# Kernel optimization log

Measured on AMD Instinct MI355X. Metric: run time of the kernel, lower is better.

Reference implementation:

```python
import jax, jax.numpy as jnp
import numpy as np

B, S, D, H = 2, 2048, 1024, 16
HD = D // H


def setup_inputs() -> dict:
    key = jax.random.key(0)
    ks = jax.random.split(key, 5)
    x = jax.random.normal(ks[0], (B, S, D), dtype=jnp.float32)
    qk_w = jax.random.normal(ks[1], (D, 2 * D), dtype=jnp.float32) * 0.02
    qk_b = jnp.zeros((2 * D,), dtype=jnp.float32)
    v_w = jax.random.normal(ks[2], (D, D), dtype=jnp.float32) * 0.02
    cproj_w = jax.random.normal(ks[3], (D, D), dtype=jnp.float32) * 0.02
    resid_gain = jnp.ones((1, H, 1, 1), dtype=jnp.float32)
    skip_gain = jnp.ones((1, H, 1, 1), dtype=jnp.float32)
    centre_gain = jnp.ones((1, H, 1, 1), dtype=jnp.float32)
    return {"x": x, "qk_w": qk_w, "qk_b": qk_b, "v_w": v_w,
            "cproj_w": cproj_w, "resid_gain": resid_gain,
            "skip_gain": skip_gain, "centre_gain": centre_gain}


def reference(x, qk_w, qk_b, v_w, cproj_w, resid_gain, skip_gain, centre_gain):
    b, s, d = x.shape
    h, hd = H, d // H
    # fused QK projection (pconv with bias)
    qk = x @ qk_w + qk_b                      # [B,S,2D]
    q, k = jnp.split(qk, 2, axis=-1)
    v = x @ v_w                               # [B,S,D] (pconv, bias=0)
    # split heads -> [B,H,S,hd]
    q = q.reshape(b, s, h, hd).transpose(0, 2, 1, 3)
    k = k.reshape(b, s, h, hd).transpose(0, 2, 1, 3)
    v = v.reshape(b, s, h, hd).transpose(0, 2, 1, 3)
    # scaled QK^T with causal mask
    scores = jnp.einsum('bhqd,bhkd->bhqk', q, k) / jnp.sqrt(jnp.float32(hd))
    causal = jnp.tril(jnp.ones((s, s), dtype=bool))
    neg = jnp.finfo(scores.dtype).min
    scores = jnp.where(causal, scores, neg)
    attn = jax.nn.softmax(scores, axis=-1)    # [B,H,S,S]
    # shaped attention: per-head resid gain + skip (identity) - centred uniform causal
    row = jnp.arange(1, s + 1, dtype=jnp.float32)
    uniform = jnp.tril(jnp.ones((s, s), dtype=jnp.float32) / row[:, None])  # [S,S]
    eye = jnp.eye(s, dtype=jnp.float32)
    new_attn = (resid_gain * attn
                + skip_gain * eye[None, None]
                - centre_gain * uniform[None, None])
    out = jnp.einsum('bhqk,bhkd->bhqd', new_attn, v)  # [B,H,S,hd]
    out = out.transpose(0, 2, 1, 3).reshape(b, s, d)  # merge heads
    out = out @ cproj_w                                # c_proj (bias=0)
    return out
```

## Files before the change

kernel.cpp:

```cpp
#include <hip/hip_runtime.h>
#include <hip/hip_bf16.h>


typedef __hip_bfloat16 bf16;
typedef short s16x8 __attribute__((ext_vector_type(8)));
typedef short s16x4 __attribute__((ext_vector_type(4)));
typedef float f32x4 __attribute__((ext_vector_type(4)));

#define NB 2
#define NS 2048
#define ND 1024
#define NH 16
#define NHD 64
#define QSCALE 0.18033688011112042f
#define THR 8.0f
#define SW(r) (((r) & 7) << 4)

__device__ __forceinline__ float b2f(unsigned short u) {
  union { float f; unsigned int i; } c; c.i = ((unsigned int)u) << 16; return c.f;
}

__device__ __forceinline__ unsigned short f2bu(float f) {
  bf16 t = __float2bfloat16(f);
  unsigned short u;
  __builtin_memcpy(&u, &t, 2);
  return u;
}

__device__ __forceinline__ void gload_lds16(const void* g, void* l) {
  __builtin_amdgcn_global_load_lds((const __attribute__((address_space(1))) void*)g,
                                   (__attribute__((address_space(3))) void*)l, 16, 0, 0);
}

__global__ __launch_bounds__(256) void cvt_bf16(const float* __restrict__ in,
                                                bf16* __restrict__ out, int n4) {
  int i = blockIdx.x * 256 + threadIdx.x;
  if (i >= n4) return;
  float4 v = ((const float4*)in)[i];
  ushort4 o;
  o.x = f2bu(v.x); o.y = f2bu(v.y); o.z = f2bu(v.z); o.w = f2bu(v.w);
  ((ushort4*)out)[i] = o;
}

__global__ __launch_bounds__(256) void tconv3(const float* __restrict__ qk_w,
                                              const float* __restrict__ v_w,
                                              const float* __restrict__ cp_w,
                                              bf16* __restrict__ qkwt,
                                              bf16* __restrict__ vwt,
                                              bf16* __restrict__ cpwt) {
  const int z = blockIdx.z;
  const int N = (z == 0) ? 2048 : 1024;
  if (blockIdx.x * 32 >= N) return;
  const float* in = (z == 0) ? qk_w : (z == 1) ? v_w : cp_w;
  bf16* out = (z == 0) ? qkwt : (z == 1) ? vwt : cpwt;
  const int K = 1024;
  __shared__ float tile[32][33];
  int nt = blockIdx.x * 32, kt = blockIdx.y * 32;
  int tx = threadIdx.x, ty = threadIdx.y;
#pragma unroll
  for (int j = 0; j < 32; j += 8)
    tile[ty + j][tx] = in[(size_t)(kt + ty + j) * N + nt + tx];
  __syncthreads();
#pragma unroll
  for (int j = 0; j < 32; j += 8)
    out[(size_t)(nt + ty + j) * K + kt + tx] = __float2bfloat16(tile[tx][ty + j]);
}

__global__ __launch_bounds__(256) void gemm_qkv(const bf16* __restrict__ A,
                                                const bf16* __restrict__ BtQK,
                                                const bf16* __restrict__ BtV,
                                                const float* __restrict__ bias,
                                                bf16* __restrict__ qo, bf16* __restrict__ ko,
                                                bf16* __restrict__ vo) {
  __shared__ alignas(16) bf16 As[128 * 32];
  __shared__ alignas(16) bf16 Bs[128 * 32];
  const int K = 1024;
  const int tid = threadIdx.x;
  const int wave = tid >> 6, lane = tid & 63;
  const int l15 = lane & 15, lg = lane >> 4;
  const int wr = wave >> 1, wc = wave & 1;
  const int brow = blockIdx.y * 128, bcol = blockIdx.x * 128;
  const bf16* Bsrc = (bcol < 2048) ? (BtQK + (size_t)bcol * K)
                                   : (BtV + (size_t)(bcol - 2048) * K);

  f32x4 acc[4][4] = {};
  const int r0 = tid >> 2;
  const int kc = (tid & 3) * 8;
  char* AsB = (char*)As;
  char* BsB = (char*)Bs;

  for (int k0 = 0; k0 < K; k0 += 32) {
    gload_lds16(A + (size_t)(brow + r0) * K + k0 + kc, AsB + tid * 16);
    gload_lds16(A + (size_t)(brow + r0 + 64) * K + k0 + kc, AsB + 4096 + tid * 16);
    gload_lds16(Bsrc + (size_t)r0 * K + k0 + kc, BsB + tid * 16);
    gload_lds16(Bsrc + (size_t)(r0 + 64) * K + k0 + kc, BsB + 4096 + tid * 16);
    __syncthreads();
    s16x8 af[4], bfr[4];
#pragma unroll
    for (int mi = 0; mi < 4; ++mi)
      af[mi] = *(const s16x8*)(As + (wr * 64 + mi * 16 + l15) * 32 + lg * 8);
#pragma unroll
    for (int ni = 0; ni < 4; ++ni)
      bfr[ni] = *(const s16x8*)(Bs + (wc * 64 + ni * 16 + l15) * 32 + lg * 8);
#pragma unroll
    for (int mi = 0; mi < 4; ++mi)
#pragma unroll
      for (int ni = 0; ni < 4; ++ni)
        acc[mi][ni] = __builtin_amdgcn_mfma_f32_16x16x32_bf16(af[mi], bfr[ni], acc[mi][ni], 0, 0, 0);
    __syncthreads();
  }

#pragma unroll
  for (int mi = 0; mi < 4; ++mi)
#pragma unroll
    for (int ni = 0; ni < 4; ++ni)
#pragma unroll
      for (int r = 0; r < 4; ++r) {
        int row = brow + wr * 64 + mi * 16 + lg * 4 + r;
        int col = bcol + wc * 64 + ni * 16 + l15;
        float v = acc[mi][ni][r];
        int b = row >> 11, s = row & 2047;
        int cc = col & 1023;
        int h = cc >> 6, e = cc & 63;
        if (col < 1024) {
          v = (v + bias[col]) * QSCALE;
          qo[((((size_t)b * NH + h) * NS) + s) * NHD + e] = __float2bfloat16(v);
        } else if (col < 2048) {
          v += bias[col];
          ko[((((size_t)b * NH + h) * NS) + s) * NHD + e] = __float2bfloat16(v);
        } else {
          vo[((((size_t)b * NH + h) * NHD) + e) * NS + s] = __float2bfloat16(v);
        }
      }
}

__global__ __launch_bounds__(256) void gemm_out(const bf16* __restrict__ A,
                                                const bf16* __restrict__ Bt,
                                                float* __restrict__ of) {
  __shared__ alignas(16) bf16 As[128 * 32];
  __shared__ alignas(16) bf16 Bs[64 * 32];
  const int K = 1024, N = 1024;
  const int tid = threadIdx.x;
  const int wave = tid >> 6, lane = tid & 63;
  const int l15 = lane & 15, lg = lane >> 4;
  const int brow = blockIdx.y * 128, bcol = blockIdx.x * 64;

  f32x4 acc[2][4] = {};
  const int r0 = tid >> 2;
  const int kc = (tid & 3) * 8;
  char* AsB = (char*)As;
  char* BsB = (char*)Bs;

  for (int k0 = 0; k0 < K; k0 += 32) {
    gload_lds16(A + (size_t)(brow + r0) * K + k0 + kc, AsB + tid * 16);
    gload_lds16(A + (size_t)(brow + r0 + 64) * K + k0 + kc, AsB + 4096 + tid * 16);
    gload_lds16(Bt + (size_t)(bcol + r0) * K + k0 + kc, BsB + tid * 16);
    __syncthreads();
    s16x8 af[2], bfr[4];
#pragma unroll
    for (int mi = 0; mi < 2; ++mi)
      af[mi] = *(const s16x8*)(As + (wave * 32 + mi * 16 + l15) * 32 + lg * 8);
#pragma unroll
    for (int ni = 0; ni < 4; ++ni)
      bfr[ni] = *(const s16x8*)(Bs + (ni * 16 + l15) * 32 + lg * 8);
#pragma unroll
    for (int mi = 0; mi < 2; ++mi)
#pragma unroll
      for (int ni = 0; ni < 4; ++ni)
        acc[mi][ni] = __builtin_amdgcn_mfma_f32_16x16x32_bf16(af[mi], bfr[ni], acc[mi][ni], 0, 0, 0);
    __syncthreads();
  }

#pragma unroll
  for (int mi = 0; mi < 2; ++mi)
#pragma unroll
    for (int ni = 0; ni < 4; ++ni)
#pragma unroll
      for (int r = 0; r < 4; ++r) {
        int row = brow + wave * 32 + mi * 16 + lg * 4 + r;
        int col = bcol + ni * 16 + l15;
        of[(size_t)row * N + col] = acc[mi][ni][r];
      }
}

__global__ __launch_bounds__(256, 4) void attn_kernel(const bf16* __restrict__ qb,
                                                      const bf16* __restrict__ kb,
                                                      const bf16* __restrict__ vtb,
                                                      const float* __restrict__ rg,
                                                      const float* __restrict__ sg,
                                                      const float* __restrict__ cg,
                                                      bf16* __restrict__ out) {
  const int hb = blockIdx.x;
  const int h = hb & 15, b = hb >> 4;
  const int qt = 31 - (int)blockIdx.y;
  const int tid = threadIdx.x, wave = tid >> 6, lane = tid & 63;
  const int l15 = lane & 15, lg = lane >> 4;

  __shared__ alignas(16) char Ks[64 * 128];
  __shared__ alignas(16) char Vs[64 * 128];
  __shared__ alignas(16) char Pl[4][2048];
  char* Plw = Pl[wave];
  const int swz = ((((l15 >> 3) ^ l15) & 7) << 4);

  const size_t hoff = ((size_t)b * NH + h) * NS * NHD;
  const bf16* Q = qb + hoff;
  const bf16* K = kb + hoff;
  const bf16* VT = vtb + hoff;
  const float rgh = rg[h], sgh = sg[h], cgh = cg[h];

  const int qbase = qt * 64 + wave * 16;
  const int qloc = wave * 16 + l15;

  s16x8 qa0 = *(const s16x8*)(Q + (size_t)(qbase + l15) * NHD + lg * 8);
  s16x8 qa1 = *(const s16x8*)(Q + (size_t)(qbase + l15) * NHD + 32 + lg * 8);

  const short ONE = 0x3F80;
  const s16x8 ones = {ONE, ONE, ONE, ONE, ONE, ONE, ONE, ONE};
  s16x8 pc0, pc1;
#pragma unroll
  for (int j = 0; j < 8; ++j) {
    pc0[j] = (lg * 8 + j <= qloc) ? ONE : (short)0;
    pc1[j] = (32 + lg * 8 + j <= qloc) ? ONE : (short)0;
  }

  f32x4 acc_o[4] = {};
  f32x4 acc_c[4] = {};
  float m_run = -INFINITY, l_run = 0.f;

  const int srow = tid >> 3;
  const int sce = (tid & 7) * 8;
  const int scb0 = (sce * 2) ^ SW(srow);
  const int scb1 = (sce * 2) ^ SW(srow + 32);

  s16x8 kra = *(const s16x8*)(K + (size_t)srow * NHD + sce);
  s16x8 krb = *(const s16x8*)(K + (size_t)(srow + 32) * NHD + sce);
  s16x8 vra = *(const s16x8*)(VT + (size_t)srow * NS + sce);
  s16x8 vrb = *(const s16x8*)(VT + (size_t)(srow + 32) * NS + sce);

  for (int t = 0; t <= qt; ++t) {
    const bool diag = (t == qt);
    __syncthreads();
    *(s16x8*)(Ks + srow * 128 + scb0) = kra;
    *(s16x8*)(Ks + (srow + 32) * 128 + scb1) = krb;
    *(s16x8*)(Vs + srow * 128 + scb0) = vra;
    *(s16x8*)(Vs + (srow + 32) * 128 + scb1) = vrb;
    if (t < qt) {
      const bf16* Kn = K + (size_t)(t + 1) * 64 * NHD;
      const bf16* Vn = VT + (t + 1) * 64;
      kra = *(const s16x8*)(Kn + (size_t)srow * NHD + sce);
      krb = *(const s16x8*)(Kn + (size_t)(srow + 32) * NHD + sce);
      vra = *(const s16x8*)(Vn + (size_t)srow * NS + sce);
      vrb = *(const s16x8*)(Vn + (size_t)(srow + 32) * NS + sce);
    }
    __syncthreads();

    f32x4 sc[4] = {};
    __builtin_amdgcn_s_setprio(1);
#pragma unroll
    for (int c = 0; c < 4; ++c) {
      const int R = c * 16 + l15;
      s16x8 kf0 = *(const s16x8*)(Ks + R * 128 + ((lg * 16) ^ SW(R)));
      s16x8 kf1 = *(const s16x8*)(Ks + R * 128 + ((64 + lg * 16) ^ SW(R)));
      sc[c] = __builtin_amdgcn_mfma_f32_16x16x32_bf16(kf0, qa0, sc[c], 0, 0, 0);
      sc[c] = __builtin_amdgcn_mfma_f32_16x16x32_bf16(kf1, qa1, sc[c], 0, 0, 0);
    }
    __builtin_amdgcn_s_setprio(0);

    if (diag) {
#pragma unroll
      for (int c = 0; c < 4; ++c)
#pragma unroll
        for (int r = 0; r < 4; ++r)
          if (c * 16 + lg * 4 + r > qloc) sc[c][r] = -INFINITY;
    }

    float mxc[4];
#pragma unroll
    for (int c = 0; c < 4; ++c)
      mxc[c] = fmaxf(fmaxf(sc[c][0], sc[c][1]), fmaxf(sc[c][2], sc[c][3]));
    float mx = fmaxf(fmaxf(mxc[0], mxc[1]), fmaxf(mxc[2], mxc[3]));
    mx = fmaxf(mx, __shfl_xor(mx, 16, 64));
    mx = fmaxf(mx, __shfl_xor(mx, 32, 64));

    const bool grow = !__all(mx <= m_run + THR);
    float m_new = grow ? fmaxf(m_run, mx) : m_run;

    float p[4][4];
    float rs = 0.f;
#pragma unroll
    for (int c = 0; c < 4; ++c)
#pragma unroll
      for (int r = 0; r < 4; ++r) {
        float e = exp2f(sc[c][r] - m_new);
        p[c][r] = e;
        rs += e;
      }
    rs += __shfl_xor(rs, 16, 64);
    rs += __shfl_xor(rs, 32, 64);

    if (grow) {
      float cr = exp2f(m_run - m_new);
      l_run = l_run * cr + rs;
      m_run = m_new;
      float crr[4];
#pragma unroll
      for (int r = 0; r < 4; ++r) crr[r] = __shfl(cr, lg * 4 + r, 64);
#pragma unroll
      for (int sub = 0; sub < 4; ++sub)
#pragma unroll
        for (int r = 0; r < 4; ++r) acc_o[sub][r] *= crr[r];
    } else {
      l_run += rs;
    }

#pragma unroll
    for (int c = 0; c < 4; ++c) {
      s16x4 pk;
      pk[0] = (short)f2bu(p[c][0]);
      pk[1] = (short)f2bu(p[c][1]);
      pk[2] = (short)f2bu(p[c][2]);
      pk[3] = (short)f2bu(p[c][3]);
      *(s16x4*)(Plw + l15 * 128 + ((c * 32 + lg * 8) ^ swz)) = pk;
    }
    s16x8 pa0 = *(const s16x8*)(Plw + l15 * 128 + ((lg * 16) ^ swz));
    s16x8 pa1 = *(const s16x8*)(Plw + l15 * 128 + ((64 + lg * 16) ^ swz));

    const s16x8 qc0 = diag ? pc0 : ones;
    const s16x8 qc1 = diag ? pc1 : ones;

    __builtin_amdgcn_s_setprio(1);
#pragma unroll
    for (int sub = 0; sub < 4; ++sub) {
      const int Rv = sub * 16 + l15;
      s16x8 vf0 = *(const s16x8*)(Vs + Rv * 128 + ((lg * 16) ^ SW(Rv)));
      s16x8 vf1 = *(const s16x8*)(Vs + Rv * 128 + ((64 + lg * 16) ^ SW(Rv)));
      acc_o[sub] = __builtin_amdgcn_mfma_f32_16x16x32_bf16(pa0, vf0, acc_o[sub], 0, 0, 0);
      acc_o[sub] = __builtin_amdgcn_mfma_f32_16x16x32_bf16(pa1, vf1, acc_o[sub], 0, 0, 0);
      acc_c[sub] = __builtin_amdgcn_mfma_f32_16x16x32_bf16(qc0, vf0, acc_c[sub], 0, 0, 0);
      acc_c[sub] = __builtin_amdgcn_mfma_f32_16x16x32_bf16(qc1, vf1, acc_c[sub], 0, 0, 0);
    }
    __builtin_amdgcn_s_setprio(0);
  }

  float linv[4];
#pragma unroll
  for (int r = 0; r < 4; ++r) linv[r] = 1.0f / __shfl(l_run, lg * 4 + r, 64);

#pragma unroll
  for (int sub = 0; sub < 4; ++sub) {
    const int d = sub * 16 + l15;
    const int cb = wave * 32 + lg * 8;
    s16x4 vr4 = *(const s16x4*)(Vs + d * 128 + (cb ^ SW(d)));
    unsigned short vbits[4];
    __builtin_memcpy(vbits, &vr4, 8);
#pragma unroll
    for (int r = 0; r < 4; ++r) {
      int q = qbase + lg * 4 + r;
      float val = rgh * acc_o[sub][r] * linv[r] + sgh * b2f(vbits[r]) -
                  cgh * acc_c[sub][r] / (float)(q + 1);
      out[((size_t)b * NS + q) * ND + h * NHD + d] = __float2bfloat16(val);
    }
  }
}

extern "C" void kernel_launch(void* const* d_in, const int* in_sizes, int n_in,
                              void* d_out, int out_size, void* d_ws, size_t ws_size,
                              hipStream_t stream) {
  const float* x = (const float*)d_in[0];
  const float* qk_w = (const float*)d_in[1];
  const float* qk_b = (const float*)d_in[2];
  const float* v_w = (const float*)d_in[3];
  const float* cproj_w = (const float*)d_in[4];
  const float* rg = (const float*)d_in[5];
  const float* sg = (const float*)d_in[6];
  const float* cg = (const float*)d_in[7];
  float* out = (float*)d_out;

  char* p = (char*)d_ws;
  bf16* xb = (bf16*)p;   p += (size_t)4096 * 1024 * 2;
  bf16* qkwt = (bf16*)p; p += (size_t)2048 * 1024 * 2;
  bf16* vwt = (bf16*)p;  p += (size_t)1024 * 1024 * 2;
  bf16* cpwt = (bf16*)p; p += (size_t)1024 * 1024 * 2;
  bf16* qbuf = (bf16*)p; p += (size_t)NB * NH * NS * NHD * 2;
  bf16* kbuf = (bf16*)p; p += (size_t)NB * NH * NS * NHD * 2;
  bf16* vtbuf = (bf16*)p; p += (size_t)NB * NH * NS * NHD * 2;
  bf16* aout = (bf16*)p; p += (size_t)4096 * 1024 * 2;

  cvt_bf16<<<4096, 256, 0, stream>>>(x, xb, (NB * NS * ND) / 4);
  tconv3<<<dim3(64, 32, 3), dim3(32, 8), 0, stream>>>(qk_w, v_w, cproj_w, qkwt, vwt, cpwt);

  gemm_qkv<<<dim3(24, 32), 256, 0, stream>>>(xb, qkwt, vwt, qk_b, qbuf, kbuf, vtbuf);
  attn_kernel<<<dim3(32, 32), 256, 0, stream>>>(qbuf, kbuf, vtbuf, rg, sg, cg, aout);
  gemm_out<<<dim3(16, 32), 256, 0, stream>>>(aout, cpwt, out);
}
```

Baseline: 132.2 us.

## Merge conversion kernels into one prologue and double-buffer attention K/V tiles

Folds the x-to-bf16 conversion and the three weight transpose-conversions into a single prologue launch, with z==0 blocks converting x, which saves one kernel launch and its drain gap. In the attention kernel, K and V shared-memory tiles become double-buffered by iteration parity, so the barrier at the top of each loop iteration is dropped and only one sync per iteration remains. Shared memory per block grows by 16 KB, which may reduce occupancy under the 4-blocks-per-CU launch bound. The final skip term now reads V from the buffer holding the diagonal tile.

```diff
diff --git a/kernel.cpp b/kernel.cpp
--- a/kernel.cpp
+++ b/kernel.cpp
@@ -32,31 +32,35 @@
                                    (__attribute__((address_space(3))) void*)l, 16, 0, 0);
 }
 
-__global__ __launch_bounds__(256) void cvt_bf16(const float* __restrict__ in,
-                                                bf16* __restrict__ out, int n4) {
-  int i = blockIdx.x * 256 + threadIdx.x;
-  if (i >= n4) return;
-  float4 v = ((const float4*)in)[i];
-  ushort4 o;
-  o.x = f2bu(v.x); o.y = f2bu(v.y); o.z = f2bu(v.z); o.w = f2bu(v.w);
-  ((ushort4*)out)[i] = o;
-}
-
-__global__ __launch_bounds__(256) void tconv3(const float* __restrict__ qk_w,
-                                              const float* __restrict__ v_w,
-                                              const float* __restrict__ cp_w,
-                                              bf16* __restrict__ qkwt,
-                                              bf16* __restrict__ vwt,
-                                              bf16* __restrict__ cpwt) {
+__global__ __launch_bounds__(256) void prologue(const float* __restrict__ x,
+                                                const float* __restrict__ qk_w,
+                                                const float* __restrict__ v_w,
+                                                const float* __restrict__ cp_w,
+                                                bf16* __restrict__ xb,
+                                                bf16* __restrict__ qkwt,
+                                                bf16* __restrict__ vwt,
+                                                bf16* __restrict__ cpwt) {
   const int z = blockIdx.z;
-  const int N = (z == 0) ? 2048 : 1024;
-  if (blockIdx.x * 32 >= N) return;
-  const float* in = (z == 0) ? qk_w : (z == 1) ? v_w : cp_w;
-  bf16* out = (z == 0) ? qkwt : (z == 1) ? vwt : cpwt;
+  const int tx = threadIdx.x, ty = threadIdx.y;
+  if (z == 0) {
+    const int lb = (int)blockIdx.x + 64 * (int)blockIdx.y;
+    const int base = lb * 2048 + (ty * 32 + tx) * 8;
+    float4 v0 = *(const float4*)(x + base);
+    float4 v1 = *(const float4*)(x + base + 4);
+    ushort4 o0, o1;
+    o0.x = f2bu(v0.x); o0.y = f2bu(v0.y); o0.z = f2bu(v0.z); o0.w = f2bu(v0.w);
+    o1.x = f2bu(v1.x); o1.y = f2bu(v1.y); o1.z = f2bu(v1.z); o1.w = f2bu(v1.w);
+    *(ushort4*)(xb + base) = o0;
+    *(ushort4*)(xb + base + 4) = o1;
+    return;
+  }
+  const int N = (z == 1) ? 2048 : 1024;
+  if ((int)blockIdx.x * 32 >= N) return;
+  const float* in = (z == 1) ? qk_w : (z == 2) ? v_w : cp_w;
+  bf16* out = (z == 1) ? qkwt : (z == 2) ? vwt : cpwt;
   const int K = 1024;
   __shared__ float tile[32][33];
   int nt = blockIdx.x * 32, kt = blockIdx.y * 32;
-  int tx = threadIdx.x, ty = threadIdx.y;
 #pragma unroll
   for (int j = 0; j < 32; j += 8)
     tile[ty + j][tx] = in[(size_t)(kt + ty + j) * N + nt + tx];
@@ -196,8 +200,8 @@
   const int tid = threadIdx.x, wave = tid >> 6, lane = tid & 63;
   const int l15 = lane & 15, lg = lane >> 4;
 
-  __shared__ alignas(16) char Ks[64 * 128];
-  __shared__ alignas(16) char Vs[64 * 128];
+  __shared__ alignas(16) char Ks[2][64 * 128];
+  __shared__ alignas(16) char Vs[2][64 * 128];
   __shared__ alignas(16) char Pl[4][2048];
   char* Plw = Pl[wave];
   const int swz = ((((l15 >> 3) ^ l15) & 7) << 4);
@@ -239,11 +243,12 @@
 
   for (int t = 0; t <= qt; ++t) {
     const bool diag = (t == qt);
-    __syncthreads();
-    *(s16x8*)(Ks + srow * 128 + scb0) = kra;
-    *(s16x8*)(Ks + (srow + 32) * 128 + scb1) = krb;
-    *(s16x8*)(Vs + srow * 128 + scb0) = vra;
-    *(s16x8*)(Vs + (srow + 32) * 128 + scb1) = vrb;
+    char* Kb = Ks[t & 1];
+    char* Vb = Vs[t & 1];
+    *(s16x8*)(Kb + srow * 128 + scb0) = kra;
+    *(s16x8*)(Kb + (srow + 32) * 128 + scb1) = krb;
+    *(s16x8*)(Vb + srow * 128 + scb0) = vra;
+    *(s16x8*)(Vb + (srow + 32) * 128 + scb1) = vrb;
     if (t < qt) {
       const bf16* Kn = K + (size_t)(t + 1) * 64 * NHD;
       const bf16* Vn = VT + (t + 1) * 64;
@@ -259,8 +264,8 @@
 #pragma unroll
     for (int c = 0; c < 4; ++c) {
       const int R = c * 16 + l15;
-      s16x8 kf0 = *(const s16x8*)(Ks + R * 128 + ((lg * 16) ^ SW(R)));
-      s16x8 kf1 = *(const s16x8*)(Ks + R * 128 + ((64 + lg * 16) ^ SW(R)));
+      s16x8 kf0 = *(const s16x8*)(Kb + R * 128 + ((lg * 16) ^ SW(R)));
+      s16x8 kf1 = *(const s16x8*)(Kb + R * 128 + ((64 + lg * 16) ^ SW(R)));
       sc[c] = __builtin_amdgcn_mfma_f32_16x16x32_bf16(kf0, qa0, sc[c], 0, 0, 0);
       sc[c] = __builtin_amdgcn_mfma_f32_16x16x32_bf16(kf1, qa1, sc[c], 0, 0, 0);
     }
@@ -332,8 +337,8 @@
 #pragma unroll
     for (int sub = 0; sub < 4; ++sub) {
       const int Rv = sub * 16 + l15;
-      s16x8 vf0 = *(const s16x8*)(Vs + Rv * 128 + ((lg * 16) ^ SW(Rv)));
-      s16x8 vf1 = *(const s16x8*)(Vs + Rv * 128 + ((64 + lg * 16) ^ SW(Rv)));
+      s16x8 vf0 = *(const s16x8*)(Vb + Rv * 128 + ((lg * 16) ^ SW(Rv)));
+      s16x8 vf1 = *(const s16x8*)(Vb + Rv * 128 + ((64 + lg * 16) ^ SW(Rv)));
       acc_o[sub] = __builtin_amdgcn_mfma_f32_16x16x32_bf16(pa0, vf0, acc_o[sub], 0, 0, 0);
       acc_o[sub] = __builtin_amdgcn_mfma_f32_16x16x32_bf16(pa1, vf1, acc_o[sub], 0, 0, 0);
       acc_c[sub] = __builtin_amdgcn_mfma_f32_16x16x32_bf16(qc0, vf0, acc_c[sub], 0, 0, 0);
@@ -342,6 +347,7 @@
     __builtin_amdgcn_s_setprio(0);
   }
 
+  const char* Vd = Vs[qt & 1];
   float linv[4];
 #pragma unroll
   for (int r = 0; r < 4; ++r) linv[r] = 1.0f / __shfl(l_run, lg * 4 + r, 64);
@@ -350,7 +356,7 @@
   for (int sub = 0; sub < 4; ++sub) {
     const int d = sub * 16 + l15;
     const int cb = wave * 32 + lg * 8;
-    s16x4 vr4 = *(const s16x4*)(Vs + d * 128 + (cb ^ SW(d)));
+    s16x4 vr4 = *(const s16x4*)(Vd + d * 128 + (cb ^ SW(d)));
     unsigned short vbits[4];
     __builtin_memcpy(vbits, &vr4, 8);
 #pragma unroll
@@ -386,9 +392,8 @@
   bf16* vtbuf = (bf16*)p; p += (size_t)NB * NH * NS * NHD * 2;
   bf16* aout = (bf16*)p; p += (size_t)4096 * 1024 * 2;
 
-  cvt_bf16<<<4096, 256, 0, stream>>>(x, xb, (NB * NS * ND) / 4);
-  tconv3<<<dim3(64, 32, 3), dim3(32, 8), 0, stream>>>(qk_w, v_w, cproj_w, qkwt, vwt, cpwt);
-
+  prologue<<<dim3(64, 32, 4), dim3(32, 8), 0, stream>>>(x, qk_w, v_w, cproj_w,
+                                                        xb, qkwt, vwt, cpwt);
   gemm_qkv<<<dim3(24, 32), 256, 0, stream>>>(xb, qkwt, vwt, qk_b, qbuf, kbuf, vtbuf);
   attn_kernel<<<dim3(32, 32), 256, 0, stream>>>(qbuf, kbuf, vtbuf, rg, sg, cg, aout);
   gemm_out<<<dim3(16, 32), 256, 0, stream>>>(aout, cpwt, out);
```

Measured after the change: 129.0 us. 2.4% less time.
